# Optimization experiments

Hardware: AMD Instinct MI355X
Metric: run time of the kernel (lower is better)

The kernel has to match this reference:

```python
import jax, jax.numpy as jnp
import numpy as np

TEMP = 0.5  # temperature
UNITS = [512, 256, 128]
B, M, D, C = 256, 512, 512, 8


def setup_inputs() -> dict:
    key = jax.random.key(0)
    ks = jax.random.split(key, 9)
    inp = {}
    inp["ec_output"] = jax.random.normal(ks[0], (B, M, D), jnp.float32)
    inp["mask"] = jax.random.randint(ks[1], (B, 1, 1, M), 0, 2).astype(jnp.float32)
    inp["label"] = jax.random.randint(ks[2], (B, C), 0, 2)
    dims = [D] + UNITS
    for i in range(3):
        fan_in = dims[i]
        inp[f"W{i+1}"] = jax.random.normal(ks[3 + i], (C, dims[i], dims[i + 1]), jnp.float32) * (1.0 / np.sqrt(fan_in))
        inp[f"b{i+1}"] = jnp.zeros((C, dims[i + 1]), jnp.float32)
    return inp


def reference(ec_output, mask, label, W1, b1, W2, b2, W3, b3):
    # masked sum pooling: mask==0 means keep (as in the TF code)
    m = (jnp.squeeze(mask) == 0).astype(ec_output.dtype)  # (B, M)
    pooled = jnp.einsum('bmd,bm->bd', ec_output, m)        # (B, D)

    # per-class 3-layer relu MLP, batched over class axis c
    h = jax.nn.relu(jnp.einsum('bd,cde->cbe', pooled, W1) + b1[:, None, :])
    h = jax.nn.relu(jnp.einsum('cbe,cef->cbf', h, W2) + b2[:, None, :])
    h = jax.nn.relu(jnp.einsum('cbf,cfg->cbg', h, W3) + b3[:, None, :])

    # tf.math.l2_normalize semantics
    z = h * jax.lax.rsqrt(jnp.maximum(jnp.sum(h * h, axis=-1, keepdims=True), 1e-12))  # (C, B, u)

    # supervised contrastive loss per class (training=True path)
    lab = label.T.astype(z.dtype)                 # (C, B)
    mask1 = (lab == 1).astype(z.dtype)
    mask0 = (lab == 0).astype(z.dtype)
    num_p = jnp.sum(mask1, axis=1, keepdims=True)  # (C, 1)
    num_n = jnp.sum(mask0, axis=1, keepdims=True)
    num_vec = num_p * mask1 + num_n * mask0        # (C, B)

    ip = jnp.einsum('cbe,cke->cbk', z, z)          # (C, B, B)
    ip = ip * (1.0 - jnp.eye(B, dtype=z.dtype)) / TEMP

    denom = num_vec * jnp.log(jnp.sum(jnp.exp(ip), axis=2))  # (C, B)
    numer = mask1 * jnp.einsum('cbk,ck->cb', ip, mask1) + mask0 * jnp.einsum('cbk,ck->cb', ip, mask0)
    losses = -jnp.sum((numer - denom) / num_vec, axis=1)      # (C,)

    return z, losses
```

## Files before the change

kernel.cpp:

```cpp
#include <hip/hip_runtime.h>
#include <hip/hip_bf16.h>

typedef unsigned short u16;
typedef __bf16 bf16x8 __attribute__((ext_vector_type(8)));
typedef float f32x4 __attribute__((ext_vector_type(4)));


__device__ __forceinline__ float bf2f(u16 u) {
    union { float f; unsigned int i; } x; x.i = ((unsigned int)u) << 16; return x.f;
}
__device__ __forceinline__ u16 f2bf(float f) {
    union { float f; unsigned int i; } x; x.f = f;
    unsigned int r = x.i + 0x7FFFu + ((x.i >> 16) & 1u);
    return (u16)(r >> 16);
}

__global__ __launch_bounds__(256) void pool_kernel(
    const u16* __restrict__ ec, const u16* __restrict__ mask,
    u16* __restrict__ pooled)
{
    int b = blockIdx.x, tid = threadIdx.x;
    __shared__ float wm[512];
    __shared__ float red[4][512];
    for (int i = 0; i < 2; i++) {
        int m = tid + i * 256;
        wm[m] = (bf2f(mask[b * 512 + m]) == 0.0f) ? 1.0f : 0.0f;
    }
    __syncthreads();
    int g = tid & 63, mo = tid >> 6;
    float acc[8];
    #pragma unroll
    for (int j = 0; j < 8; j++) acc[j] = 0.0f;
    const u16* base = ec + (size_t)b * 512 * 512;
    for (int m = mo; m < 512; m += 4) {
        if (wm[m] != 0.0f) {
            union { uint4 v; u16 s[8]; } u;
            u.v = *(const uint4*)&base[(size_t)m * 512 + g * 8];
            #pragma unroll
            for (int j = 0; j < 8; j++) acc[j] += bf2f(u.s[j]);
        }
    }
    #pragma unroll
    for (int j = 0; j < 8; j++) red[mo][g * 8 + j] = acc[j];
    __syncthreads();
    for (int i = 0; i < 2; i++) {
        int d = tid + i * 256;
        float s = red[0][d] + red[1][d] + red[2][d] + red[3][d];
        pooled[(size_t)b * 512 + d] = f2bf(s);
    }
}

__global__ __launch_bounds__(256) void mlp_gemm64(
    const u16* __restrict__ A, const u16* __restrict__ W,
    const u16* __restrict__ bias, u16* __restrict__ out,
    int K, int N, int aBatch, int mtiles, int ntiles)
{
    int bid = blockIdx.x;
    int per_c = mtiles * ntiles;
    int c = bid / per_c, rem = bid % per_c;
    int mt = rem / ntiles, nt = rem % ntiles;
    const u16* aBase = A + (size_t)c * aBatch + (size_t)mt * 64 * K;
    const u16* wBase = W + (size_t)c * K * N + nt * 64;
    __shared__ __align__(16) u16 As[64][72];
    __shared__ __align__(16) u16 Bs[64][72];
    int tid = threadIdx.x;
    int w = tid >> 6, l15 = tid & 15, q = (tid >> 4) & 3;
    f32x4 acc[4];
    #pragma unroll
    for (int t = 0; t < 4; t++)
        #pragma unroll
        for (int e = 0; e < 4; e++) acc[t][e] = 0.0f;

    for (int k0 = 0; k0 < K; k0 += 64) {
        #pragma unroll
        for (int i = 0; i < 2; i++) {
            int idx = tid + i * 256;
            int r = idx >> 3, kc = idx & 7;
            *(uint4*)&As[r][kc * 8] = *(const uint4*)&aBase[(size_t)r * K + k0 + kc * 8];
            int kk = idx >> 3, n8 = (idx & 7) * 8;
            union { uint4 v; u16 s[8]; } u;
            u.v = *(const uint4*)&wBase[(size_t)(k0 + kk) * N + n8];
            #pragma unroll
            for (int j = 0; j < 8; j++) Bs[n8 + j][kk] = u.s[j];
        }
        __syncthreads();
        #pragma unroll
        for (int ks = 0; ks < 64; ks += 32) {
            bf16x8 av = *(const bf16x8*)&As[w * 16 + l15][ks + q * 8];
            #pragma unroll
            for (int t = 0; t < 4; t++) {
                bf16x8 bv = *(const bf16x8*)&Bs[t * 16 + l15][ks + q * 8];
                acc[t] = __builtin_amdgcn_mfma_f32_16x16x32_bf16(av, bv, acc[t], 0, 0, 0);
            }
        }
        __syncthreads();
    }
    #pragma unroll
    for (int t = 0; t < 4; t++) {
        int col = nt * 64 + t * 16 + l15;
        float bv = bf2f(bias[c * N + col]);
        #pragma unroll
        for (int r = 0; r < 4; r++) {
            int row = mt * 64 + w * 16 + q * 4 + r;
            float v = acc[t][r] + bv;
            v = v > 0.0f ? v : 0.0f;
            out[((size_t)c * 256 + row) * N + col] = f2bf(v);
        }
    }
}

__global__ __launch_bounds__(256) void mlp_gemm3_norm(
    const u16* __restrict__ A, const u16* __restrict__ W,
    const u16* __restrict__ bias, float* __restrict__ zout, u16* __restrict__ zbf)
{
    const int K = 256, N = 128;
    int bid = blockIdx.x;
    int c = bid >> 2, mt = bid & 3;
    const u16* aBase = A + ((size_t)c * 256 + mt * 64) * K;
    const u16* wBase = W + (size_t)c * K * N;
    __shared__ __align__(16) u16 As[64][72];
    __shared__ __align__(16) u16 Bs[128][72];
    int tid = threadIdx.x;
    int w = tid >> 6, l15 = tid & 15, q = (tid >> 4) & 3;
    f32x4 acc[8];
    #pragma unroll
    for (int t = 0; t < 8; t++)
        #pragma unroll
        for (int e = 0; e < 4; e++) acc[t][e] = 0.0f;

    for (int k0 = 0; k0 < K; k0 += 64) {
        #pragma unroll
        for (int i = 0; i < 2; i++) {
            int idx = tid + i * 256; int r = idx >> 3, kc = idx & 7;
            *(uint4*)&As[r][kc * 8] = *(const uint4*)&aBase[(size_t)r * K + k0 + kc * 8];
        }
        #pragma unroll
        for (int i = 0; i < 4; i++) {
            int idx = tid + i * 256;
            int kk = idx >> 4, n8 = (idx & 15) * 8;
            union { uint4 v; u16 s[8]; } u;
            u.v = *(const uint4*)&wBase[(size_t)(k0 + kk) * N + n8];
            #pragma unroll
            for (int j = 0; j < 8; j++) Bs[n8 + j][kk] = u.s[j];
        }
        __syncthreads();
        #pragma unroll
        for (int ks = 0; ks < 64; ks += 32) {
            bf16x8 av = *(const bf16x8*)&As[w * 16 + l15][ks + q * 8];
            #pragma unroll
            for (int t = 0; t < 8; t++) {
                bf16x8 bv = *(const bf16x8*)&Bs[t * 16 + l15][ks + q * 8];
                acc[t] = __builtin_amdgcn_mfma_f32_16x16x32_bf16(av, bv, acc[t], 0, 0, 0);
            }
        }
        __syncthreads();
    }
    float val[8][4];
    float ssq[4] = {0.f, 0.f, 0.f, 0.f};
    #pragma unroll
    for (int t = 0; t < 8; t++) {
        float bv = bf2f(bias[c * N + t * 16 + l15]);
        #pragma unroll
        for (int r = 0; r < 4; r++) {
            float v = acc[t][r] + bv;
            v = v > 0.0f ? v : 0.0f;
            val[t][r] = v;
            ssq[r] += v * v;
        }
    }
    #pragma unroll
    for (int off = 1; off < 16; off <<= 1)
        #pragma unroll
        for (int r = 0; r < 4; r++) ssq[r] += __shfl_xor(ssq[r], off);
    float sc[4];
    #pragma unroll
    for (int r = 0; r < 4; r++) sc[r] = rsqrtf(fmaxf(ssq[r], 1e-12f));
    #pragma unroll
    for (int t = 0; t < 8; t++)
        #pragma unroll
        for (int r = 0; r < 4; r++) {
            int row = mt * 64 + w * 16 + q * 4 + r;
            int col = t * 16 + l15;
            float zv = val[t][r] * sc[r];
            size_t o = ((size_t)c * 256 + row) * 128 + col;
            zout[o] = zv;
            zbf[o] = f2bf(zv);
        }
}

__global__ __launch_bounds__(256) void contrast_partial(
    const u16* __restrict__ z, const int* __restrict__ label,
    float* __restrict__ rws, float* __restrict__ s1ws, float* __restrict__ s0ws)
{
    int bid = blockIdx.x;
    int c = bid >> 4, rem = bid & 15;
    int bt = rem >> 2, kt = rem & 3;
    __shared__ __align__(16) u16 Zb[64][136];
    __shared__ __align__(16) u16 Zk[64][136];
    __shared__ float lm1[64];
    int tid = threadIdx.x;
    int w = tid >> 6, l15 = tid & 15, q = (tid >> 4) & 3;
    const u16* zc = z + (size_t)c * 256 * 128;
    #pragma unroll
    for (int i = 0; i < 4; i++) {
        int idx = tid + i * 256; int r = idx >> 4, kc = idx & 15;
        *(uint4*)&Zb[r][kc * 8] = *(const uint4*)&zc[(size_t)(bt * 64 + r) * 128 + kc * 8];
        *(uint4*)&Zk[r][kc * 8] = *(const uint4*)&zc[(size_t)(kt * 64 + r) * 128 + kc * 8];
    }
    if (tid < 64) lm1[tid] = (label[(kt * 64 + tid) * 8 + c] == 1) ? 1.0f : 0.0f;
    __syncthreads();

    f32x4 acc[4];
    #pragma unroll
    for (int t = 0; t < 4; t++)
        #pragma unroll
        for (int e = 0; e < 4; e++) acc[t][e] = 0.0f;
    #pragma unroll
    for (int ks = 0; ks < 128; ks += 32) {
        bf16x8 av = *(const bf16x8*)&Zb[w * 16 + l15][ks + q * 8];
        #pragma unroll
        for (int t = 0; t < 4; t++) {
            bf16x8 bv = *(const bf16x8*)&Zk[t * 16 + l15][ks + q * 8];
            acc[t] = __builtin_amdgcn_mfma_f32_16x16x32_bf16(av, bv, acc[t], 0, 0, 0);
        }
    }
    float pr[4] = {0.f,0.f,0.f,0.f}, p1[4] = {0.f,0.f,0.f,0.f}, p0[4] = {0.f,0.f,0.f,0.f};
    #pragma unroll
    for (int t = 0; t < 4; t++) {
        int kl = t * 16 + l15;
        int kkg = kt * 64 + kl;
        float m1 = lm1[kl];
        #pragma unroll
        for (int r = 0; r < 4; r++) {
            int rbg = bt * 64 + w * 16 + q * 4 + r;
            float v = (rbg == kkg) ? 0.0f : acc[t][r] * 2.0f;
            pr[r] += __expf(v);
            p1[r] += v * m1;
            p0[r] += v * (1.0f - m1);
        }
    }
    #pragma unroll
    for (int off = 1; off < 16; off <<= 1)
        #pragma unroll
        for (int r = 0; r < 4; r++) {
            pr[r] += __shfl_xor(pr[r], off);
            p1[r] += __shfl_xor(p1[r], off);
            p0[r] += __shfl_xor(p0[r], off);
        }
    if (l15 == 0) {
        #pragma unroll
        for (int r = 0; r < 4; r++) {
            int rbg = bt * 64 + w * 16 + q * 4 + r;
            atomicAdd(&rws[c * 256 + rbg], pr[r]);
            atomicAdd(&s1ws[c * 256 + rbg], p1[r]);
            atomicAdd(&s0ws[c * 256 + rbg], p0[r]);
        }
    }
}

__global__ __launch_bounds__(256) void loss_kernel(
    const int* __restrict__ label, const float* __restrict__ rws,
    const float* __restrict__ s1ws, const float* __restrict__ s0ws,
    float* __restrict__ lout)
{
    int c = blockIdx.x, b = threadIdx.x;
    __shared__ float sh[256];
    int lab = label[b * 8 + c];
    float m1 = (lab == 1) ? 1.0f : 0.0f;
    sh[b] = m1;
    __syncthreads();
    for (int s = 128; s > 0; s >>= 1) {
        if (b < s) sh[b] += sh[b + s];
        __syncthreads();
    }
    float num_p = sh[0];
    __syncthreads();
    float num_n = 256.0f - num_p;
    float num_vec = (m1 > 0.0f) ? num_p : num_n;
    float numer = (m1 > 0.0f) ? s1ws[c * 256 + b] : s0ws[c * 256 + b];
    float term = numer / num_vec - __logf(rws[c * 256 + b]);
    sh[b] = term;
    __syncthreads();
    for (int s = 128; s > 0; s >>= 1) {
        if (b < s) sh[b] += sh[b + s];
        __syncthreads();
    }
    if (b == 0) lout[c] = -sh[0];
}

extern "C" void kernel_launch(void* const* d_in, const int* in_sizes, int n_in,
                              void* d_out, int out_size, void* d_ws, size_t ws_size,
                              hipStream_t stream) {
    (void)in_sizes; (void)n_in; (void)ws_size;
    const u16* ec   = (const u16*)d_in[0];
    const u16* mask = (const u16*)d_in[1];
    const int* label = (const int*)d_in[2];
    const u16* W1 = (const u16*)d_in[3];
    const u16* b1 = (const u16*)d_in[4];
    const u16* W2 = (const u16*)d_in[5];
    const u16* b2 = (const u16*)d_in[6];
    const u16* W3 = (const u16*)d_in[7];
    const u16* b3 = (const u16*)d_in[8];
    float* zout = (float*)d_out;
    char* ws = (char*)d_ws;
    u16* pooled = (u16*)(ws + 0);
    u16* h1     = (u16*)(ws + 262144);
    u16* h2     = (u16*)(ws + 2359296);
    u16* zbf    = (u16*)(ws + 3407872);
    float* rws  = (float*)(ws + 3932160);
    float* s1ws = rws + 2048;
    float* s0ws = rws + 4096;

    hipMemsetAsync(rws, 0, 3 * 2048 * sizeof(float), stream);
    pool_kernel<<<256, 256, 0, stream>>>(ec, mask, pooled);
    mlp_gemm64<<<256, 256, 0, stream>>>(pooled, W1, b1, h1, 512, 512, 0, 4, 8);
    mlp_gemm64<<<128, 256, 0, stream>>>(h1, W2, b2, h2, 512, 256, 256 * 512, 4, 4);
    mlp_gemm3_norm<<<32, 256, 0, stream>>>(h2, W3, b3, zout, zbf);
    contrast_partial<<<128, 256, 0, stream>>>(zbf, label, rws, s1ws, s0ws);
    loss_kernel<<<8, 256, 0, stream>>>(label, rws, s1ws, s0ws, zout + (out_size - 8));
}
```

Measured before the change: 444.4 us.

## Widen pooling blocks, double-buffer MLP GEMM tiles, split final GEMM rows

Result: faster. 384.8 us (-13.4%).

```diff
diff --git a/kernel.cpp b/kernel.cpp
--- a/kernel.cpp
+++ b/kernel.cpp
@@ -15,24 +15,22 @@
     return (u16)(r >> 16);
 }
 
-__global__ __launch_bounds__(256) void pool_kernel(
+__global__ __launch_bounds__(1024) void pool_kernel(
     const u16* __restrict__ ec, const u16* __restrict__ mask,
     u16* __restrict__ pooled)
 {
     int b = blockIdx.x, tid = threadIdx.x;
     __shared__ float wm[512];
-    __shared__ float red[4][512];
-    for (int i = 0; i < 2; i++) {
-        int m = tid + i * 256;
-        wm[m] = (bf2f(mask[b * 512 + m]) == 0.0f) ? 1.0f : 0.0f;
-    }
+    __shared__ float red[16][512];
+    if (tid < 512)
+        wm[tid] = (bf2f(mask[b * 512 + tid]) == 0.0f) ? 1.0f : 0.0f;
     __syncthreads();
     int g = tid & 63, mo = tid >> 6;
     float acc[8];
     #pragma unroll
     for (int j = 0; j < 8; j++) acc[j] = 0.0f;
     const u16* base = ec + (size_t)b * 512 * 512;
-    for (int m = mo; m < 512; m += 4) {
+    for (int m = mo; m < 512; m += 16) {
         if (wm[m] != 0.0f) {
             union { uint4 v; u16 s[8]; } u;
             u.v = *(const uint4*)&base[(size_t)m * 512 + g * 8];
@@ -43,10 +41,11 @@
     #pragma unroll
     for (int j = 0; j < 8; j++) red[mo][g * 8 + j] = acc[j];
     __syncthreads();
-    for (int i = 0; i < 2; i++) {
-        int d = tid + i * 256;
-        float s = red[0][d] + red[1][d] + red[2][d] + red[3][d];
-        pooled[(size_t)b * 512 + d] = f2bf(s);
+    if (tid < 512) {
+        float s = 0.0f;
+        #pragma unroll
+        for (int k = 0; k < 16; k++) s += red[k][tid];
+        pooled[(size_t)b * 512 + tid] = f2bf(s);
     }
 }
 
@@ -61,39 +60,56 @@
     int mt = rem / ntiles, nt = rem % ntiles;
     const u16* aBase = A + (size_t)c * aBatch + (size_t)mt * 64 * K;
     const u16* wBase = W + (size_t)c * K * N + nt * 64;
-    __shared__ __align__(16) u16 As[64][72];
-    __shared__ __align__(16) u16 Bs[64][72];
+    __shared__ __align__(16) u16 As[2][64][72];
+    __shared__ __align__(16) u16 Bs[2][64][72];
     int tid = threadIdx.x;
     int w = tid >> 6, l15 = tid & 15, q = (tid >> 4) & 3;
+    int r0 = tid >> 3, kc0 = tid & 7;
+    int r1 = (tid + 256) >> 3, kc1 = tid & 7;
     f32x4 acc[4];
     #pragma unroll
     for (int t = 0; t < 4; t++)
         #pragma unroll
         for (int e = 0; e < 4; e++) acc[t][e] = 0.0f;
 
-    for (int k0 = 0; k0 < K; k0 += 64) {
-        #pragma unroll
-        for (int i = 0; i < 2; i++) {
-            int idx = tid + i * 256;
-            int r = idx >> 3, kc = idx & 7;
-            *(uint4*)&As[r][kc * 8] = *(const uint4*)&aBase[(size_t)r * K + k0 + kc * 8];
-            int kk = idx >> 3, n8 = (idx & 7) * 8;
-            union { uint4 v; u16 s[8]; } u;
-            u.v = *(const uint4*)&wBase[(size_t)(k0 + kk) * N + n8];
-            #pragma unroll
-            for (int j = 0; j < 8; j++) Bs[n8 + j][kk] = u.s[j];
+    uint4 aReg[2], wReg[2];
+    aReg[0] = *(const uint4*)&aBase[(size_t)r0 * K + kc0 * 8];
+    aReg[1] = *(const uint4*)&aBase[(size_t)r1 * K + kc1 * 8];
+    wReg[0] = *(const uint4*)&wBase[(size_t)r0 * N + kc0 * 8];
+    wReg[1] = *(const uint4*)&wBase[(size_t)r1 * N + kc1 * 8];
+
+    int nIter = K >> 6;
+    for (int it = 0; it < nIter; ++it) {
+        int cur = it & 1;
+        *(uint4*)&As[cur][r0][kc0 * 8] = aReg[0];
+        *(uint4*)&As[cur][r1][kc1 * 8] = aReg[1];
+        {
+            union { uint4 v; u16 s[8]; } u; u.v = wReg[0];
+            #pragma unroll
+            for (int j = 0; j < 8; j++) Bs[cur][kc0 * 8 + j][r0] = u.s[j];
+        }
+        {
+            union { uint4 v; u16 s[8]; } u; u.v = wReg[1];
+            #pragma unroll
+            for (int j = 0; j < 8; j++) Bs[cur][kc1 * 8 + j][r1] = u.s[j];
+        }
+        if (it + 1 < nIter) {
+            int k0n = (it + 1) * 64;
+            aReg[0] = *(const uint4*)&aBase[(size_t)r0 * K + k0n + kc0 * 8];
+            aReg[1] = *(const uint4*)&aBase[(size_t)r1 * K + k0n + kc1 * 8];
+            wReg[0] = *(const uint4*)&wBase[(size_t)(k0n + r0) * N + kc0 * 8];
+            wReg[1] = *(const uint4*)&wBase[(size_t)(k0n + r1) * N + kc1 * 8];
         }
         __syncthreads();
         #pragma unroll
         for (int ks = 0; ks < 64; ks += 32) {
-            bf16x8 av = *(const bf16x8*)&As[w * 16 + l15][ks + q * 8];
+            bf16x8 av = *(const bf16x8*)&As[cur][w * 16 + l15][ks + q * 8];
             #pragma unroll
             for (int t = 0; t < 4; t++) {
-                bf16x8 bv = *(const bf16x8*)&Bs[t * 16 + l15][ks + q * 8];
+                bf16x8 bv = *(const bf16x8*)&Bs[cur][t * 16 + l15][ks + q * 8];
                 acc[t] = __builtin_amdgcn_mfma_f32_16x16x32_bf16(av, bv, acc[t], 0, 0, 0);
             }
         }
-        __syncthreads();
     }
     #pragma unroll
     for (int t = 0; t < 4; t++) {
@@ -115,23 +131,24 @@
 {
     const int K = 256, N = 128;
     int bid = blockIdx.x;
-    int c = bid >> 2, mt = bid & 3;
-    const u16* aBase = A + ((size_t)c * 256 + mt * 64) * K;
+    int c = bid >> 4, mt = bid & 15;
+    const u16* aBase = A + ((size_t)c * 256 + mt * 16) * K;
     const u16* wBase = W + (size_t)c * K * N;
-    __shared__ __align__(16) u16 As[64][72];
+    __shared__ __align__(16) u16 As[16][72];
     __shared__ __align__(16) u16 Bs[128][72];
+    __shared__ float ssq_s[4][16];
+    __shared__ float scale_s[16];
     int tid = threadIdx.x;
     int w = tid >> 6, l15 = tid & 15, q = (tid >> 4) & 3;
-    f32x4 acc[8];
-    #pragma unroll
-    for (int t = 0; t < 8; t++)
+    f32x4 acc[2];
+    #pragma unroll
+    for (int t = 0; t < 2; t++)
         #pragma unroll
         for (int e = 0; e < 4; e++) acc[t][e] = 0.0f;
 
     for (int k0 = 0; k0 < K; k0 += 64) {
-        #pragma unroll
-        for (int i = 0; i < 2; i++) {
-            int idx = tid + i * 256; int r = idx >> 3, kc = idx & 7;
+        if (tid < 128) {
+            int r = tid >> 3, kc = tid & 7;
             *(uint4*)&As[r][kc * 8] = *(const uint4*)&aBase[(size_t)r * K + k0 + kc * 8];
         }
         #pragma unroll
@@ -146,20 +163,20 @@
         __syncthreads();
         #pragma unroll
         for (int ks = 0; ks < 64; ks += 32) {
-            bf16x8 av = *(const bf16x8*)&As[w * 16 + l15][ks + q * 8];
-            #pragma unroll
-            for (int t = 0; t < 8; t++) {
-                bf16x8 bv = *(const bf16x8*)&Bs[t * 16 + l15][ks + q * 8];
+            bf16x8 av = *(const bf16x8*)&As[l15][ks + q * 8];
+            #pragma unroll
+            for (int t = 0; t < 2; t++) {
+                bf16x8 bv = *(const bf16x8*)&Bs[w * 32 + t * 16 + l15][ks + q * 8];
                 acc[t] = __builtin_amdgcn_mfma_f32_16x16x32_bf16(av, bv, acc[t], 0, 0, 0);
             }
         }
         __syncthreads();
     }
-    float val[8][4];
+    float val[2][4];
     float ssq[4] = {0.f, 0.f, 0.f, 0.f};
     #pragma unroll
-    for (int t = 0; t < 8; t++) {
-        float bv = bf2f(bias[c * N + t * 16 + l15]);
+    for (int t = 0; t < 2; t++) {
+        float bv = bf2f(bias[c * N + w * 32 + t * 16 + l15]);
         #pragma unroll
         for (int r = 0; r < 4; r++) {
             float v = acc[t][r] + bv;
@@ -172,16 +189,23 @@
     for (int off = 1; off < 16; off <<= 1)
         #pragma unroll
         for (int r = 0; r < 4; r++) ssq[r] += __shfl_xor(ssq[r], off);
-    float sc[4];
-    #pragma unroll
-    for (int r = 0; r < 4; r++) sc[r] = rsqrtf(fmaxf(ssq[r], 1e-12f));
-    #pragma unroll
-    for (int t = 0; t < 8; t++)
-        #pragma unroll
-        for (int r = 0; r < 4; r++) {
-            int row = mt * 64 + w * 16 + q * 4 + r;
-            int col = t * 16 + l15;
-            float zv = val[t][r] * sc[r];
+    if (l15 == 0) {
+        #pragma unroll
+        for (int r = 0; r < 4; r++) ssq_s[w][q * 4 + r] = ssq[r];
+    }
+    __syncthreads();
+    if (tid < 16) {
+        float s = ssq_s[0][tid] + ssq_s[1][tid] + ssq_s[2][tid] + ssq_s[3][tid];
+        scale_s[tid] = rsqrtf(fmaxf(s, 1e-12f));
+    }
+    __syncthreads();
+    #pragma unroll
+    for (int t = 0; t < 2; t++)
+        #pragma unroll
+        for (int r = 0; r < 4; r++) {
+            int row = mt * 16 + q * 4 + r;
+            int col = w * 32 + t * 16 + l15;
+            float zv = val[t][r] * scale_s[q * 4 + r];
             size_t o = ((size_t)c * 256 + row) * 128 + col;
             zout[o] = zv;
             zbf[o] = f2bf(zv);
@@ -312,10 +336,10 @@
     float* s0ws = rws + 4096;
 
     hipMemsetAsync(rws, 0, 3 * 2048 * sizeof(float), stream);
-    pool_kernel<<<256, 256, 0, stream>>>(ec, mask, pooled);
+    pool_kernel<<<256, 1024, 0, stream>>>(ec, mask, pooled);
     mlp_gemm64<<<256, 256, 0, stream>>>(pooled, W1, b1, h1, 512, 512, 0, 4, 8);
     mlp_gemm64<<<128, 256, 0, stream>>>(h1, W2, b2, h2, 512, 256, 256 * 512, 4, 4);
-    mlp_gemm3_norm<<<32, 256, 0, stream>>>(h2, W3, b3, zout, zbf);
+    mlp_gemm3_norm<<<128, 256, 0, stream>>>(h2, W3, b3, zout, zbf);
     contrast_partial<<<128, 256, 0, stream>>>(zbf, label, rws, s1ws, s0ws);
     loss_kernel<<<8, 256, 0, stream>>>(label, rws, s1ws, s0ws, zout + (out_size - 8));
 }
```
